# Kernel tuning notes

Measured on AMD Instinct MI355X. Metric: run time of the kernel, lower is better.

The kernel has to match this reference:

```python
import jax, jax.numpy as jnp
import numpy as np

NUM_NODES = 100000
NUM_EDGES = 3200000
N_PER = 400            # nodes per graph (equal-size graphs)
NUM_GRAPHS = 250
K = 100                # sort-pooling k
DIM = 32
IN_DIM = 128
TOTAL = 3 * DIM + 1    # 97 = concat channel count
GDIM = 128
OUT_DIM = 2
DENSE_DIM = (((K - 2) // 2 + 1) - 5 + 1) * 64  # 46*64 = 2944


def setup_inputs() -> dict:
    key = jax.random.key(0)
    ks = jax.random.split(key, 12)

    def lin(k, shape, fan_in):
        return jax.random.normal(k, shape, jnp.float32) / np.float32(np.sqrt(fan_in))

    return {
        "x": jax.random.normal(ks[0], (NUM_NODES, IN_DIM), jnp.float32),
        "edge_index": jax.random.randint(ks[1], (2, NUM_EDGES), 0, NUM_NODES, dtype=jnp.int32),
        "batch": jnp.arange(NUM_NODES, dtype=jnp.int32) // N_PER,
        "W1": lin(ks[2], (IN_DIM, DIM), IN_DIM), "b1": jnp.zeros((DIM,), jnp.float32),
        "W2": lin(ks[3], (DIM, DIM), DIM),       "b2": jnp.zeros((DIM,), jnp.float32),
        "W3": lin(ks[4], (DIM, DIM), DIM),       "b3": jnp.zeros((DIM,), jnp.float32),
        "W4": lin(ks[5], (DIM, 1), DIM),         "b4": jnp.zeros((1,), jnp.float32),
        "cw1": lin(ks[6], (128, 1, TOTAL), TOTAL),   "cb1": jnp.zeros((128,), jnp.float32),
        "cw2": lin(ks[7], (64, 128, 5), 128 * 5),    "cb2": jnp.zeros((64,), jnp.float32),
        "fw1": lin(ks[8], (GDIM, DENSE_DIM), DENSE_DIM), "fb1": jnp.zeros((GDIM,), jnp.float32),
        "fw3": lin(ks[9], (OUT_DIM, GDIM), GDIM),        "fb3": jnp.zeros((OUT_DIM,), jnp.float32),
    }


def _gcn(h_in, W, b, src, dst, coef, deg_inv):
    # GCNConv (improved=False): D^{-1/2}(A+I)D^{-1/2} (h W) + b
    h = h_in @ W
    agg = jax.ops.segment_sum(h[src] * coef, dst, num_segments=NUM_NODES)
    return agg + h * deg_inv[:, None] + b  # deg_inv = self-loop norm dis[i]^2


def reference(x, edge_index, batch, W1, b1, W2, b2, W3, b3, W4, b4,
              cw1, cb1, cw2, cb2, fw1, fb1, fw3, fb3):
    src, dst = edge_index[0], edge_index[1]
    deg = jax.ops.segment_sum(jnp.ones((NUM_EDGES,), x.dtype), dst, num_segments=NUM_NODES) + 1.0
    dis = jax.lax.rsqrt(deg)
    coef = (dis[src] * dis[dst])[:, None]
    deg_inv = 1.0 / deg

    x1 = jnp.tanh(_gcn(x,  W1, b1, src, dst, coef, deg_inv))
    x2 = jnp.tanh(_gcn(x1, W2, b2, src, dst, coef, deg_inv))
    x3 = jnp.tanh(_gcn(x2, W3, b3, src, dst, coef, deg_inv))
    x4 = jnp.tanh(_gcn(x2, W4, b4, src, dst, coef, deg_inv))  # NB: conv4 consumes x2 (as in source)
    xc = jnp.concatenate([x1, x2, x3, x4], axis=1)  # [N, 97]

    # global_sort_pool: per-graph descending sort by last channel, keep top K nodes
    order = jnp.lexsort((-xc[:, -1], batch))  # primary: graph id, secondary: -last channel
    xs = xc[order].reshape(NUM_GRAPHS, N_PER, TOTAL)[:, :K]  # [B, K, 97]

    # Conv1d(1, 128, kernel=stride=97) over flattened [B,1,K*97] == per-slot linear map
    c1 = jax.nn.relu(jnp.einsum('bkt,ct->bck', xs, cw1[:, 0, :]) + cb1[None, :, None])  # [B,128,K]
    p1 = c1.reshape(NUM_GRAPHS, 128, K // 2, 2).max(axis=-1)  # MaxPool1d(2,2) -> [B,128,50]
    c2 = jax.lax.conv_general_dilated(p1, cw2, (1,), 'VALID',
                                      dimension_numbers=('NCH', 'OIH', 'NCH'))
    c2 = jax.nn.relu(c2 + cb2[None, :, None])  # [B,64,46]

    flat = c2.reshape(NUM_GRAPHS, -1)            # [B, 2944]
    h = jax.nn.relu(flat @ fw1.T + fb1)          # fc1 + relu (dropout = identity in eval)
    logits = h @ fw3.T + fb3                     # fc3
    return jax.nn.log_softmax(logits, axis=-1)
```

## Files before the change

### kernel.cpp

```cpp
#include <hip/hip_runtime.h>
#include <hip/hip_bf16.h>

#define NNODES 100000
#define NEDGES 3200000
#define NPADE  4000000
#define NPER   400
#define NGRAPH 250
#define KTOP   100
#define DIM    32
#define INDIM  128
#define TOTALC 97
#define BSHIFT 7
#define BNODES 128
#define NBUCK  782
#define NCHUNK 200
#define CHSZ   16000

__device__ __forceinline__ float bf(unsigned short u) {
    return __uint_as_float(((unsigned)u) << 16);
}
__device__ __forceinline__ unsigned short f2bf(float f) {
    unsigned u = __float_as_uint(f);
    unsigned r = ((u >> 16) & 1u) + 0x7FFFu;
    return (unsigned short)((u + r) >> 16);
}

#define OW_W1   0
#define OW_B1   4096
#define OW_W2   4128
#define OW_B2   5152
#define OW_W3   5184
#define OW_B3   6208
#define OW_W4   6240
#define OW_B4   6272
#define OW_CW1  6280
#define OW_CB1  18696
#define OW_CW2  18824
#define OW_CB2  59784
#define OW_FW1  59848
#define OW_FB1  436680
#define OW_FW3  436808
#define OW_FB3  437064
#define OW_TOT  437072

struct Srcs { const void* p[16]; };

__global__ void k_setup(const unsigned int* __restrict__ xw, Srcs sr,
                        float* __restrict__ dst, float* __restrict__ fw1t,
                        float* __restrict__ w2t8, int* __restrict__ flag) {
    __shared__ int cs[256];
    int t = threadIdx.x;
    int c = 0;
    for (int i = t; i < 4096; i += 256) {
        unsigned e = (xw[i] >> 23) & 0xFFu;
        if (e >= 100u && e <= 150u) c++;
    }
    cs[t] = c;
    __syncthreads();
    for (int off = 128; off > 0; off >>= 1) {
        if (t < off) cs[t] += cs[t + off];
        __syncthreads();
    }
    int isb = (cs[0] < 2048) ? 1 : 0;
    if (blockIdx.x == 0 && t == 0) flag[0] = isb;
    long idx = (long)blockIdx.x * 256 + t;
    if (idx < OW_TOT) {
        const int st[16] = {OW_W1, OW_B1, OW_W2, OW_B2, OW_W3, OW_B3, OW_W4, OW_B4,
                            OW_CW1, OW_CB1, OW_CW2, OW_CB2, OW_FW1, OW_FB1, OW_FW3, OW_FB3};
        const int nn[16] = {4096, 32, 1024, 32, 1024, 32, 32, 1,
                            12416, 128, 40960, 64, 376832, 128, 256, 2};
        #pragma unroll
        for (int s = 0; s < 16; s++) {
            if (idx >= st[s] && idx < st[s] + nn[s]) {
                int l = (int)idx - st[s];
                dst[idx] = isb ? bf(((const unsigned short*)sr.p[s])[l])
                               : ((const float*)sr.p[s])[l];
            }
        }
    } else if (idx < OW_TOT + 376832) {
        int i2 = (int)(idx - OW_TOT);
        float v = isb ? bf(((const unsigned short*)sr.p[12])[i2])
                      : ((const float*)sr.p[12])[i2];
        int j = i2 / 2944, d = i2 - j * 2944;
        fw1t[d * 128 + j] = v;
    } else if (idx < OW_TOT + 376832 + 65536) {
        int k = (int)(idx - OW_TOT - 376832);
        int q = k & 7;
        int co = k >> 3;
        int cc = co >> 6, o = co & 63;
        float v = 0.f;
        if (q < 5) {
            int si = (o * 128 + cc) * 5 + q;
            v = isb ? bf(((const unsigned short*)sr.p[10])[si])
                    : ((const float*)sr.p[10])[si];
        }
        w2t8[k] = v;
    }
}


__global__ __launch_bounds__(1024) void k_hist(const int* __restrict__ ei, int* __restrict__ ghist) {
    __shared__ int h[NBUCK];
    int c = blockIdx.x, t = threadIdx.x;
    for (int i = t; i < NBUCK; i += 1024) h[i] = 0;
    __syncthreads();
    int base = c * CHSZ;
    for (int e = base + t; e < base + CHSZ; e += 1024)
        atomicAdd(&h[ei[NEDGES + e] >> BSHIFT], 1);
    __syncthreads();
    for (int i = t; i < NBUCK; i += 1024) ghist[i * NCHUNK + c] = h[i];
}

__global__ __launch_bounds__(256) void k_scanChunk(int* __restrict__ ghist, int* __restrict__ bcnt) {
    __shared__ int s[256];
    int b = blockIdx.x, t = threadIdx.x;
    int v = (t < NCHUNK) ? ghist[b * NCHUNK + t] : 0;
    s[t] = v;
    __syncthreads();
    for (int o = 1; o < 256; o <<= 1) {
        int u = (t >= o) ? s[t - o] : 0;
        __syncthreads();
        s[t] += u;
        __syncthreads();
    }
    if (t < NCHUNK) ghist[b * NCHUNK + t] = s[t] - v;
    if (t == NCHUNK - 1) bcnt[b] = s[t];
}

__global__ void k_scanB(const int* __restrict__ bcnt, int* __restrict__ boff) {
    __shared__ int s[1024];
    int t = threadIdx.x;
    int v = (t < NBUCK) ? bcnt[t] : 0;
    s[t] = v;
    __syncthreads();
    for (int o = 1; o < 1024; o <<= 1) {
        int u = (t >= o) ? s[t - o] : 0;
        __syncthreads();
        s[t] += u;
        __syncthreads();
    }
    if (t < NBUCK) boff[t] = s[t] - v;
}

__global__ __launch_bounds__(1024) void k_binwrite(const int* __restrict__ ei, const int* __restrict__ boff,
                           const int* __restrict__ ghist, unsigned* __restrict__ staged) {
    __shared__ int cur[NBUCK];
    int c = blockIdx.x, t = threadIdx.x;
    for (int i = t; i < NBUCK; i += 1024) cur[i] = boff[i] + ghist[i * NCHUNK + c];
    __syncthreads();
    int base = c * CHSZ;
    for (int e = base + t; e < base + CHSZ; e += 1024) {
        int s = ei[e], d = ei[NEDGES + e];
        int b = d >> BSHIFT;
        int pos = atomicAdd(&cur[b], 1);
        staged[pos] = ((unsigned)(d & (BNODES - 1)) << 17) | (unsigned)s;
    }
}

__global__ __launch_bounds__(256) void k_nodecnt(const unsigned* __restrict__ staged,
                          const int* __restrict__ boff, int* __restrict__ degi) {
    __shared__ int cnt[BNODES];
    int b = blockIdx.x, t = threadIdx.x;
    if (t < BNODES) cnt[t] = 0;
    __syncthreads();
    int s0 = boff[b];
    int s1 = (b + 1 < NBUCK) ? boff[b + 1] : NEDGES;
    for (int i = s0 + t; i < s1; i += 256)
        atomicAdd(&cnt[staged[i] >> 17], 1);
    __syncthreads();
    int n0 = b << BSHIFT;
    int nn = min(BNODES, NNODES - n0);
    if (t < nn) degi[n0 + t] = cnt[t];
}

__global__ void k_bsum(const int* __restrict__ degi, float* __restrict__ dis,
                       float* __restrict__ dinv, int* __restrict__ bsums) {
    __shared__ int s[256];
    int t = threadIdx.x;
    int i = blockIdx.x * 256 + t;
    int dg = (i < NNODES) ? degi[i] : 0;
    if (i < NNODES) {
        float d = (float)(dg + 1);
        dis[i]  = rsqrtf(d);
        dinv[i] = 1.0f / d;
    }
    s[t] = (i < NNODES) ? ((dg + 7) & ~7) : 0;
    __syncthreads();
    for (int off = 128; off > 0; off >>= 1) {
        if (t < off) s[t] += s[t + off];
        __syncthreads();
    }
    if (t == 0) bsums[blockIdx.x] = s[0];
}

__global__ void k_scanb(int* __restrict__ bsums, int nb) {
    __shared__ int s[512];
    int t = threadIdx.x;
    int v = (t < nb) ? bsums[t] : 0;
    s[t] = v;
    __syncthreads();
    for (int off = 1; off < 512; off <<= 1) {
        int u = (t >= off) ? s[t - off] : 0;
        __syncthreads();
        s[t] += u;
        __syncthreads();
    }
    if (t < nb) bsums[t] = s[t] - v;
}

__global__ void k_scanf(const int* __restrict__ degi, const int* __restrict__ bsums,
                        int* __restrict__ row_off) {
    __shared__ int s[256];
    int t = threadIdx.x;
    int i = blockIdx.x * 256 + t;
    int v = (i < NNODES) ? ((degi[i] + 7) & ~7) : 0;
    s[t] = v;
    __syncthreads();
    for (int off = 1; off < 256; off <<= 1) {
        int u = (t >= off) ? s[t - off] : 0;
        __syncthreads();
        s[t] += u;
        __syncthreads();
    }
    if (i < NNODES) row_off[i] = bsums[blockIdx.x] + s[t] - v;
}

__global__ __launch_bounds__(256) void k_csrfix(const unsigned* __restrict__ staged,
                         const int* __restrict__ boff, const int* __restrict__ row_off,
                         const float* __restrict__ dis,
                         int* __restrict__ csr_src, float* __restrict__ csr_cf) {
    __shared__ int cnt[BNODES];
    __shared__ int rofs[BNODES];
    __shared__ float disl[BNODES];
    int b = blockIdx.x, t = threadIdx.x;
    int n0 = b << BSHIFT;
    int nn = min(BNODES, NNODES - n0);
    if (t < BNODES) {
        cnt[t]  = 0;
        rofs[t] = (t < nn) ? row_off[n0 + t] : 0;
        disl[t] = (t < nn) ? dis[n0 + t] : 0.f;
    }
    __syncthreads();
    int s0 = boff[b];
    int s1 = (b + 1 < NBUCK) ? boff[b + 1] : NEDGES;
    for (int i = s0 + t; i < s1; i += 256) {
        unsigned rec = staged[i];
        int dl = rec >> 17, s = rec & 0x1FFFF;
        int r = atomicAdd(&cnt[dl], 1);
        int slot = rofs[dl] + r;
        csr_src[slot] = s;
        csr_cf[slot]  = dis[s] * disl[dl];
    }
    __syncthreads();
    if (t < nn) {
        int d = cnt[t], dp = (d + 7) & ~7;
        for (int s2 = d; s2 < dp; s2++) {
            csr_src[rofs[t] + s2] = 0;
            csr_cf[rofs[t] + s2]  = 0.f;
        }
    }
}


__global__ void k_mm1(const void* __restrict__ xraw, const float* __restrict__ W1f,
                      const int* __restrict__ flag, float* __restrict__ h) {
    __shared__ float w[INDIM * DIM];
    __shared__ float xsh[8 * INDIM];
    int t = threadIdx.x;
    for (int i = t; i < INDIM * DIM; i += 256) w[i] = W1f[i];
    if (flag[0]) {
        const unsigned int* xsrc = (const unsigned int*)((const unsigned short*)xraw
                                   + (size_t)blockIdx.x * 8 * INDIM);
        for (int i = t; i < 512; i += 256) {
            unsigned u = xsrc[i];
            xsh[2 * i]     = __uint_as_float(u << 16);
            xsh[2 * i + 1] = __uint_as_float(u & 0xFFFF0000u);
        }
    } else {
        const float4* xsrc = (const float4*)((const float*)xraw + (size_t)blockIdx.x * 8 * INDIM);
        float4* xdst = (float4*)xsh;
        for (int i = t; i < 256; i += 256) xdst[i] = xsrc[i];
    }
    __syncthreads();
    int ln = t >> 5, c = t & 31;
    const float* xr = xsh + ln * INDIM;
    float acc = 0.f;
    #pragma unroll 8
    for (int j = 0; j < INDIM; j++) acc += xr[j] * w[j * DIM + c];
    h[(size_t)blockIdx.x * 256 + t] = acc;
}

__global__ void k_gather(const float* __restrict__ xin, const float* __restrict__ h4in,
                         const int* __restrict__ csr_src, const float* __restrict__ csr_cf,
                         const int* __restrict__ row_off, const int* __restrict__ degi,
                         const float* __restrict__ dinv,
                         const float* __restrict__ Wm,
                         const float* __restrict__ bias,
                         const float* __restrict__ w4v,
                         const float* __restrict__ b4,
                         float* __restrict__ xout, float* __restrict__ x4out,
                         float* __restrict__ h4out) {
    __shared__ float wsh[DIM * DIM];
    __shared__ float w4sh[DIM];
    __shared__ float zsh[8 * DIM];
    __shared__ float osh[8 * DIM];
    int t = threadIdx.x;
    if (Wm)  for (int i = t; i < DIM * DIM; i += 256) wsh[i] = Wm[i];
    if (w4v && t < DIM) w4sh[t] = w4v[t];
    int node = blockIdx.x * 8 + (t >> 5);
    int lane = t & 31;
    int wg   = t >> 5;
    int start = row_off[node];
    int cnt   = degi[node];
    int iters = (cnt + 7) >> 3;
    const int4*   ip = (const int4*)(csr_src + start);
    const float4* cp = (const float4*)(csr_cf + start);
    float acc0 = 0.f, acc1 = 0.f;
    if (iters > 0) {
        int4   iA = ip[0], iB = ip[1];
        float4 cA = cp[0], cB = cp[1];
        for (int k = 1; k < iters; k++) {
            int4   nA = ip[2 * k],     nB = ip[2 * k + 1];
            float4 dA = cp[2 * k],     dB = cp[2 * k + 1];
            acc0 += xin[(size_t)iA.x * DIM + lane] * cA.x;
            acc1 += xin[(size_t)iA.y * DIM + lane] * cA.y;
            acc0 += xin[(size_t)iA.z * DIM + lane] * cA.z;
            acc1 += xin[(size_t)iA.w * DIM + lane] * cA.w;
            acc0 += xin[(size_t)iB.x * DIM + lane] * cB.x;
            acc1 += xin[(size_t)iB.y * DIM + lane] * cB.y;
            acc0 += xin[(size_t)iB.z * DIM + lane] * cB.z;
            acc1 += xin[(size_t)iB.w * DIM + lane] * cB.w;
            iA = nA; iB = nB; cA = dA; cB = dB;
        }
        acc0 += xin[(size_t)iA.x * DIM + lane] * cA.x;
        acc1 += xin[(size_t)iA.y * DIM + lane] * cA.y;
        acc0 += xin[(size_t)iA.z * DIM + lane] * cA.z;
        acc1 += xin[(size_t)iA.w * DIM + lane] * cA.w;
        acc0 += xin[(size_t)iB.x * DIM + lane] * cB.x;
        acc1 += xin[(size_t)iB.y * DIM + lane] * cB.y;
        acc0 += xin[(size_t)iB.z * DIM + lane] * cB.z;
        acc1 += xin[(size_t)iB.w * DIM + lane] * cB.w;
    }
    float di = dinv[node];
    float z = acc0 + acc1 + xin[(size_t)node * DIM + lane] * di;
    if (!Wm) {
        xout[(size_t)node * DIM + lane] = tanhf(z + bias[lane]);
    } else {
        zsh[wg * DIM + lane] = z;
        __syncthreads();
        const float* zr = zsh + wg * DIM;
        float a = bias[lane];
        #pragma unroll
        for (int j = 0; j < DIM; j++) a += zr[j] * wsh[j * DIM + lane];
        float outv = tanhf(a);
        xout[(size_t)node * DIM + lane] = outv;
        if (h4out) {
            osh[wg * DIM + lane] = outv;
            __syncthreads();
            if (lane == 0) {
                const float* xr = osh + wg * DIM;
                float a4 = 0.f;
                #pragma unroll
                for (int j = 0; j < DIM; j++) a4 += xr[j] * w4sh[j];
                h4out[node] = a4;
            }
        }
    }
    if (h4in) {
        int cntp = iters << 3;
        float a4 = 0.f;
        for (int ee = lane; ee < cntp; ee += 32)
            a4 += h4in[csr_src[start + ee]] * csr_cf[start + ee];
        for (int off = 16; off > 0; off >>= 1) a4 += __shfl_xor(a4, off, 32);
        if (lane == 0) x4out[node] = tanhf(a4 + h4in[node] * di + b4[0]);
    }
}

__global__ __launch_bounds__(1024) void
k_sortconv1(const float* __restrict__ x1, const float* __restrict__ x2,
            const float* __restrict__ x3, const float* __restrict__ x4,
            const float* __restrict__ cw1f, const float* __restrict__ cb1f,
            float* __restrict__ p1g) {
    __shared__ unsigned long long keys[512];
    __shared__ __align__(16) float xs[32 * 100];
    __shared__ __align__(16) float ws[32 * 128];
    __shared__ int nsh[KTOP];
    int g = blockIdx.x, t = threadIdx.x;
    for (int i = t; i < 512; i += 1024) {
        unsigned long long kk = 0xFFFFFFFFFFFFFFFFULL;
        if (i < NPER) {
            unsigned u = __float_as_uint(x4[g * NPER + i]);
            u = (u & 0x80000000u) ? ~u : (u | 0x80000000u);
            kk = ((unsigned long long)(~u) << 32) | (unsigned)i;
        }
        keys[i] = kk;
    }
    __syncthreads();
    for (int k = 2; k <= 512; k <<= 1)
        for (int j = k >> 1; j > 0; j >>= 1) {
            for (int i = t; i < 512; i += 1024) {
                int l = i ^ j;
                if (l > i) {
                    unsigned long long a = keys[i], b = keys[l];
                    bool asc = ((i & k) == 0);
                    if ((a > b) == asc) { keys[i] = b; keys[l] = a; }
                }
            }
            __syncthreads();
        }
    if (t < KTOP) nsh[t] = g * NPER + (int)(unsigned)(keys[t] & 0xFFFFFFFFu);
    int ct = (t & 31) * 4;
    int kt = (t >> 5) * 4;
    bool act = (t < 800);
    float acc[4][4] = {};
    for (int ch = 0; ch < 3; ch++) {
        const float* arr = (ch == 0) ? x1 : (ch == 1) ? x2 : x3;
        __syncthreads();
        for (int i = t; i < 3200; i += 1024) {
            int q = i & 31, k = i >> 5;
            xs[q * 100 + k] = arr[(size_t)nsh[k] * 32 + q];
        }
        for (int i = t; i < 4096; i += 1024) {
            int c = i & 127, q = i >> 7;
            ws[q * 128 + c] = cw1f[c * TOTALC + ch * 32 + q];
        }
        __syncthreads();
        if (act) {
            for (int q = 0; q < 32; q++) {
                float4 wv = *(const float4*)&ws[q * 128 + ct];
                float4 xv = *(const float4*)&xs[q * 100 + kt];
                float xa[4] = { xv.x, xv.y, xv.z, xv.w };
                float wa[4] = { wv.x, wv.y, wv.z, wv.w };
                #pragma unroll
                for (int a = 0; a < 4; a++)
                    #pragma unroll
                    for (int b = 0; b < 4; b++)
                        acc[a][b] += xa[a] * wa[b];
            }
        }
    }
    if (act) {
        float wa[4];
        #pragma unroll
        for (int b = 0; b < 4; b++) wa[b] = cw1f[(ct + b) * TOTALC + 96];
        #pragma unroll
        for (int a = 0; a < 4; a++) {
            float xv = x4[nsh[kt + a]];
            #pragma unroll
            for (int b = 0; b < 4; b++) acc[a][b] += xv * wa[b];
        }
        int jbase = kt >> 1;
        #pragma unroll
        for (int b = 0; b < 4; b++) {
            float bias = cb1f[ct + b];
            float m0 = fmaxf(fmaxf(acc[0][b], acc[1][b]) + bias, 0.f);
            float m1 = fmaxf(fmaxf(acc[2][b], acc[3][b]) + bias, 0.f);
            p1g[((size_t)g * 128 + ct + b) * 50 + jbase]     = m0;
            p1g[((size_t)g * 128 + ct + b) * 50 + jbase + 1] = m1;
        }
    }
}

__global__ __launch_bounds__(512) void
k_conv2(const float* __restrict__ p1g, const float* __restrict__ w2t8,
        const float* __restrict__ cb2f, float* __restrict__ flatg) {
    __shared__ __align__(16) float p1s[128 * 52];
    __shared__ float fl[64 * 25];
    int bid = blockIdx.x;
    int g = bid >> 1, ph = bid & 1;
    int t = threadIdx.x;
    int p0 = ph ? 24 : 0;
    int np = ph ? 22 : 24;
    for (int i = t; i < 128 * 50; i += 512) {
        int c = i / 50, p = i % 50;
        p1s[c * 52 + p] = p1g[(size_t)g * 6400 + i];
    }
    for (int i = t; i < 128 * 2; i += 512) {
        int c = i >> 1;
        p1s[c * 52 + 50 + (i & 1)] = 0.f;
    }
    for (int i = t; i < 64 * 25; i += 512) fl[i] = 0.f;
    __syncthreads();
    {
        int o = t & 63;
        int c8 = t >> 6;
        float acc[24];
        #pragma unroll
        for (int p = 0; p < 24; p++) acc[p] = 0.f;
        int cbeg = c8 * 16;
        for (int c = cbeg; c < cbeg + 16; c++) {
            const float4* wb = (const float4*)(w2t8 + (((size_t)c * 64 + o) << 3));
            float4 wA = wb[0], wB = wb[1];
            float w0 = wA.x, w1 = wA.y, w2 = wA.z, w3 = wA.w, w4 = wB.x;
            float win[28];
            const float4* wsrc = (const float4*)&p1s[c * 52 + p0];
            #pragma unroll
            for (int v = 0; v < 7; v++) {
                float4 f = wsrc[v];
                win[4 * v] = f.x; win[4 * v + 1] = f.y; win[4 * v + 2] = f.z; win[4 * v + 3] = f.w;
            }
            #pragma unroll
            for (int p = 0; p < 24; p++)
                acc[p] += win[p] * w0 + win[p + 1] * w1 + win[p + 2] * w2
                        + win[p + 3] * w3 + win[p + 4] * w4;
        }
        for (int p = 0; p < np; p++) atomicAdd(&fl[o * 25 + p], acc[p]);
    }
    __syncthreads();
    for (int i = t; i < 64 * 24; i += 512) {
        int o = i / 24, p = i - o * 24;
        if (p < np)
            flatg[(size_t)g * 2944 + o * 46 + p0 + p] = fmaxf(fl[o * 25 + p] + cb2f[o], 0.f);
    }
}

__global__ __launch_bounds__(1024) void
k_fc1(const float* __restrict__ flatg, const float* __restrict__ fw1t,
      float* __restrict__ hpart) {
    __shared__ float fls[5 * 368];
    __shared__ float hp[8 * 5 * 128];
    int b = blockIdx.x;
    int gt = b >> 3, kt = b & 7;
    int t = threadIdx.x;
    int g0 = gt * 5;
    int d0 = kt * 368;
    for (int i = t; i < 5 * 368; i += 1024) {
        int g = i / 368, dd = i - g * 368;
        fls[i] = flatg[(size_t)(g0 + g) * 2944 + d0 + dd];
    }
    __syncthreads();
    int og = t & 127, s8 = t >> 7;
    int ds = s8 * 46;
    const float* wp = fw1t + (size_t)(d0 + ds) * 128 + og;
    const float* f0 = fls + ds;
    float a0 = 0.f, a1 = 0.f, a2 = 0.f, a3 = 0.f, a4 = 0.f;
    #pragma unroll 2
    for (int d = 0; d < 46; d++) {
        float w = wp[(size_t)d * 128];
        a0 += f0[d]            * w;
        a1 += f0[368 + d]      * w;
        a2 += f0[2 * 368 + d]  * w;
        a3 += f0[3 * 368 + d]  * w;
        a4 += f0[4 * 368 + d]  * w;
    }
    hp[(s8 * 5 + 0) * 128 + og] = a0;
    hp[(s8 * 5 + 1) * 128 + og] = a1;
    hp[(s8 * 5 + 2) * 128 + og] = a2;
    hp[(s8 * 5 + 3) * 128 + og] = a3;
    hp[(s8 * 5 + 4) * 128 + og] = a4;
    __syncthreads();
    if (t < 640) {
        int g = t >> 7, o2 = t & 127;
        float s = 0.f;
        #pragma unroll
        for (int s2 = 0; s2 < 8; s2++) s += hp[(s2 * 5 + g) * 128 + o2];
        hpart[((size_t)kt * NGRAPH + g0 + g) * 128 + o2] = s;
    }
}

__global__ void k_fc3(const float* __restrict__ hpart, const float* __restrict__ fb1f,
                      const float* __restrict__ fw3f, const float* __restrict__ fb3f,
                      const int* __restrict__ flag, void* __restrict__ outp) {
    __shared__ float hsh[128];
    int g = blockIdx.x, t = threadIdx.x;
    float s = fb1f[t];
    #pragma unroll
    for (int kt = 0; kt < 8; kt++) s += hpart[((size_t)kt * NGRAPH + g) * 128 + t];
    hsh[t] = fmaxf(s, 0.f);
    __syncthreads();
    if (t < 64) {
        float h0 = hsh[t], h1 = hsh[t + 64];
        float l0 = h0 * fw3f[t] + h1 * fw3f[t + 64];
        float l1 = h0 * fw3f[128 + t] + h1 * fw3f[192 + t];
        #pragma unroll
        for (int off = 32; off > 0; off >>= 1) {
            l0 += __shfl_down(l0, off, 64);
            l1 += __shfl_down(l1, off, 64);
        }
        if (t == 0) {
            l0 += fb3f[0]; l1 += fb3f[1];
            float m = fmaxf(l0, l1);
            float lse = m + logf(expf(l0 - m) + expf(l1 - m));
            if (flag[0]) {
                unsigned short* ob = (unsigned short*)outp;
                ob[g * 2 + 0] = f2bf(l0 - lse);
                ob[g * 2 + 1] = f2bf(l1 - lse);
            } else {
                float* of = (float*)outp;
                of[g * 2 + 0] = l0 - lse;
                of[g * 2 + 1] = l1 - lse;
            }
        }
    }
}


extern "C" void kernel_launch(void* const* d_in, const int* in_sizes, int n_in,
                              void* d_out, int out_size, void* d_ws, size_t ws_size,
                              hipStream_t stream) {
    const void* x  = d_in[0];
    const int* ei  = (const int*)d_in[1];

    char* p = (char*)d_ws;
    auto alloc = [&](size_t bytes) -> void* {
        void* r = (void*)p;
        p += (bytes + 255) & ~(size_t)255;
        return r;
    };
    int*      flag    = (int*)alloc(256);
    float*    wcv     = (float*)alloc((size_t)OW_TOT * 4);
    float*    fw1t    = (float*)alloc((size_t)376832 * 4);
    int*      ghist   = (int*)alloc((size_t)NBUCK * NCHUNK * 4);
    int*      bcnt    = (int*)alloc(1024 * 4);
    int*      boff    = (int*)alloc(1024 * 4);
    int*      bsums   = (int*)alloc(512 * 4);
    int*      degi    = (int*)alloc((size_t)NNODES * 4);
    int*      row_off = (int*)alloc((size_t)NNODES * 4);
    float*    dis     = (float*)alloc((size_t)NNODES * 4);
    float*    dinv    = (float*)alloc((size_t)NNODES * 4);
    unsigned* staged  = (unsigned*)alloc((size_t)NEDGES * 4);
    int*      csr_src = (int*)alloc((size_t)NPADE * 4);
    float*    csr_cf  = (float*)alloc((size_t)NPADE * 4);
    float*    hbuf    = (float*)alloc((size_t)NNODES * DIM * 4);
    float*    h4buf   = (float*)alloc((size_t)NNODES * 4);
    float*    x1      = (float*)alloc((size_t)NNODES * DIM * 4);
    float*    x2      = (float*)alloc((size_t)NNODES * DIM * 4);
    float*    x3      = (float*)alloc((size_t)NNODES * DIM * 4);
    float*    x4      = (float*)alloc((size_t)NNODES * 4);
    float*    p1g     = (float*)alloc((size_t)NGRAPH * 128 * 50 * 4);
    float*    w2t     = (float*)alloc((size_t)64 * 128 * 8 * 4);
    float*    flatg   = (float*)alloc((size_t)NGRAPH * 2944 * 4);
    float*    hpart   = (float*)alloc((size_t)8 * NGRAPH * 128 * 4);
    (void)in_sizes; (void)n_in; (void)out_size; (void)ws_size;

    Srcs sr;
    for (int i = 0; i < 16; i++) sr.p[i] = d_in[3 + i];
    k_setup<<<3436, 256, 0, stream>>>((const unsigned int*)x, sr, wcv, fw1t, w2t, flag);

    k_hist     <<<NCHUNK, 1024, 0, stream>>>(ei, ghist);
    k_scanChunk<<<NBUCK, 256, 0, stream>>>(ghist, bcnt);
    k_scanB    <<<1, 1024, 0, stream>>>(bcnt, boff);
    k_binwrite <<<NCHUNK, 1024, 0, stream>>>(ei, boff, ghist, staged);
    k_nodecnt  <<<NBUCK, 256, 0, stream>>>(staged, boff, degi);
    k_bsum     <<<391, 256, 0, stream>>>(degi, dis, dinv, bsums);
    k_scanb    <<<1, 512, 0, stream>>>(bsums, 391);
    k_scanf    <<<391, 256, 0, stream>>>(degi, bsums, row_off);
    k_csrfix   <<<NBUCK, 256, 0, stream>>>(staged, boff, row_off, dis, csr_src, csr_cf);

    k_mm1   <<<12500, 256, 0, stream>>>(x, wcv + OW_W1, flag, hbuf);
    k_gather<<<12500, 256, 0, stream>>>(hbuf, nullptr, csr_src, csr_cf, row_off, degi, dinv,
                                        nullptr, wcv + OW_B1, nullptr, nullptr,
                                        x1, nullptr, nullptr);
    k_gather<<<12500, 256, 0, stream>>>(x1, nullptr, csr_src, csr_cf, row_off, degi, dinv,
                                        wcv + OW_W2, wcv + OW_B2, wcv + OW_W4, nullptr,
                                        x2, nullptr, h4buf);
    k_gather<<<12500, 256, 0, stream>>>(x2, h4buf, csr_src, csr_cf, row_off, degi, dinv,
                                        wcv + OW_W3, wcv + OW_B3, nullptr, wcv + OW_B4,
                                        x3, x4, nullptr);

    k_sortconv1<<<NGRAPH, 1024, 0, stream>>>(x1, x2, x3, x4, wcv + OW_CW1, wcv + OW_CB1, p1g);
    k_conv2    <<<2 * NGRAPH, 512, 0, stream>>>(p1g, w2t, wcv + OW_CB2, flatg);
    k_fc1      <<<400, 1024, 0, stream>>>(flatg, fw1t, hpart);
    k_fc3      <<<NGRAPH, 128, 0, stream>>>(hpart, wcv + OW_FB1, wcv + OW_FW3, wcv + OW_FB3,
                                            flag, d_out);
}
```

Baseline: 580.6 us.

## Fold GCN edge coefficients into pre-scaled features and drop per-edge coefficient array

Factors the symmetric normalisation dis[src]*dis[dst] out of the edge loop by storing node features pre-scaled by dis[src] and multiplying by dis[dst] after aggregation. The per-edge coefficient array is removed, so each gather reads only source indices. Padding slots now point to an extra zero row instead of carrying a zero weight. The degree/row-offset scans are merged into the bucket kernels, which cuts several launches. In exchange, sort-pool has to undo the scaling with a stored sqrt(deg) for x1 and x2, which adds small rounding differences.

Result: faster. 525.8 us (median of 2 runs) (-9.4%).

```diff
diff --git a/kernel.cpp b/kernel.cpp
--- a/kernel.cpp
+++ b/kernel.cpp
@@ -47,7 +47,9 @@
 
 __global__ void k_setup(const unsigned int* __restrict__ xw, Srcs sr,
                         float* __restrict__ dst, float* __restrict__ fw1t,
-                        float* __restrict__ w2t8, int* __restrict__ flag) {
+                        float* __restrict__ w2t8, int* __restrict__ flag,
+                        float* __restrict__ hb, float* __restrict__ x1b,
+                        float* __restrict__ x2b, float* __restrict__ h4b) {
     __shared__ int cs[256];
     int t = threadIdx.x;
     int c = 0;
@@ -62,7 +64,15 @@
         __syncthreads();
     }
     int isb = (cs[0] < 2048) ? 1 : 0;
-    if (blockIdx.x == 0 && t == 0) flag[0] = isb;
+    if (blockIdx.x == 0) {
+        if (t == 0) flag[0] = isb;
+        if (t < 32) {
+            hb[(size_t)NNODES * DIM + t]  = 0.f;
+            x1b[(size_t)NNODES * DIM + t] = 0.f;
+            x2b[(size_t)NNODES * DIM + t] = 0.f;
+        }
+        if (t == 32) h4b[NNODES] = 0.f;
+    }
     long idx = (long)blockIdx.x * 256 + t;
     if (idx < OW_TOT) {
         const int st[16] = {OW_W1, OW_B1, OW_W2, OW_B2, OW_W3, OW_B3, OW_W4, OW_B4,
@@ -127,10 +137,10 @@
     if (t == NCHUNK - 1) bcnt[b] = s[t];
 }
 
-__global__ void k_scanB(const int* __restrict__ bcnt, int* __restrict__ boff) {
+__global__ void k_scanB(const int* __restrict__ in, int* __restrict__ out) {
     __shared__ int s[1024];
     int t = threadIdx.x;
-    int v = (t < NBUCK) ? bcnt[t] : 0;
+    int v = (t < NBUCK) ? in[t] : 0;
     s[t] = v;
     __syncthreads();
     for (int o = 1; o < 1024; o <<= 1) {
@@ -139,7 +149,7 @@
         s[t] += u;
         __syncthreads();
     }
-    if (t < NBUCK) boff[t] = s[t] - v;
+    if (t < NBUCK) out[t] = s[t] - v;
 }
 
 __global__ __launch_bounds__(1024) void k_binwrite(const int* __restrict__ ei, const int* __restrict__ boff,
@@ -158,8 +168,11 @@
 }
 
 __global__ __launch_bounds__(256) void k_nodecnt(const unsigned* __restrict__ staged,
-                          const int* __restrict__ boff, int* __restrict__ degi) {
+                          const int* __restrict__ boff, int* __restrict__ degi,
+                          float* __restrict__ dis, float* __restrict__ rdis,
+                          int* __restrict__ bucksum) {
     __shared__ int cnt[BNODES];
+    __shared__ int ps[256];
     int b = blockIdx.x, t = threadIdx.x;
     if (t < BNODES) cnt[t] = 0;
     __syncthreads();
@@ -170,76 +183,43 @@
     __syncthreads();
     int n0 = b << BSHIFT;
     int nn = min(BNODES, NNODES - n0);
-    if (t < nn) degi[n0 + t] = cnt[t];
-}
-
-__global__ void k_bsum(const int* __restrict__ degi, float* __restrict__ dis,
-                       float* __restrict__ dinv, int* __restrict__ bsums) {
-    __shared__ int s[256];
-    int t = threadIdx.x;
-    int i = blockIdx.x * 256 + t;
-    int dg = (i < NNODES) ? degi[i] : 0;
-    if (i < NNODES) {
+    int dg = (t < nn) ? cnt[t] : 0;
+    if (t < nn) {
+        degi[n0 + t] = dg;
         float d = (float)(dg + 1);
-        dis[i]  = rsqrtf(d);
-        dinv[i] = 1.0f / d;
-    }
-    s[t] = (i < NNODES) ? ((dg + 7) & ~7) : 0;
+        dis[n0 + t]  = rsqrtf(d);
+        rdis[n0 + t] = sqrtf(d);
+    }
+    ps[t] = (t < nn) ? ((dg + 7) & ~7) : 0;
     __syncthreads();
     for (int off = 128; off > 0; off >>= 1) {
-        if (t < off) s[t] += s[t + off];
-        __syncthreads();
-    }
-    if (t == 0) bsums[blockIdx.x] = s[0];
-}
-
-__global__ void k_scanb(int* __restrict__ bsums, int nb) {
-    __shared__ int s[512];
-    int t = threadIdx.x;
-    int v = (t < nb) ? bsums[t] : 0;
-    s[t] = v;
-    __syncthreads();
-    for (int off = 1; off < 512; off <<= 1) {
-        int u = (t >= off) ? s[t - off] : 0;
-        __syncthreads();
-        s[t] += u;
-        __syncthreads();
-    }
-    if (t < nb) bsums[t] = s[t] - v;
-}
-
-__global__ void k_scanf(const int* __restrict__ degi, const int* __restrict__ bsums,
-                        int* __restrict__ row_off) {
-    __shared__ int s[256];
-    int t = threadIdx.x;
-    int i = blockIdx.x * 256 + t;
-    int v = (i < NNODES) ? ((degi[i] + 7) & ~7) : 0;
-    s[t] = v;
-    __syncthreads();
-    for (int off = 1; off < 256; off <<= 1) {
-        int u = (t >= off) ? s[t - off] : 0;
-        __syncthreads();
-        s[t] += u;
-        __syncthreads();
-    }
-    if (i < NNODES) row_off[i] = bsums[blockIdx.x] + s[t] - v;
+        if (t < off) ps[t] += ps[t + off];
+        __syncthreads();
+    }
+    if (t == 0) bucksum[b] = ps[0];
 }
 
 __global__ __launch_bounds__(256) void k_csrfix(const unsigned* __restrict__ staged,
-                         const int* __restrict__ boff, const int* __restrict__ row_off,
-                         const float* __restrict__ dis,
-                         int* __restrict__ csr_src, float* __restrict__ csr_cf) {
+                         const int* __restrict__ boff, const int* __restrict__ buckoff,
+                         const int* __restrict__ degi,
+                         int* __restrict__ csr_src, int* __restrict__ row_off) {
     __shared__ int cnt[BNODES];
+    __shared__ int sc[BNODES];
     __shared__ int rofs[BNODES];
-    __shared__ float disl[BNODES];
     int b = blockIdx.x, t = threadIdx.x;
     int n0 = b << BSHIFT;
     int nn = min(BNODES, NNODES - n0);
-    if (t < BNODES) {
-        cnt[t]  = 0;
-        rofs[t] = (t < nn) ? row_off[n0 + t] : 0;
-        disl[t] = (t < nn) ? dis[n0 + t] : 0.f;
-    }
+    int pd = (t < nn) ? ((degi[n0 + t] + 7) & ~7) : 0;
+    if (t < BNODES) { cnt[t] = 0; sc[t] = pd; }
+    __syncthreads();
+    for (int o = 1; o < BNODES; o <<= 1) {
+        int u = (t >= o && t < BNODES) ? sc[t - o] : 0;
+        __syncthreads();
+        if (t < BNODES) sc[t] += u;
+        __syncthreads();
+    }
+    if (t < BNODES) rofs[t] = buckoff[b] + sc[t] - pd;
+    if (t < nn) row_off[n0 + t] = rofs[t];
     __syncthreads();
     int s0 = boff[b];
     int s1 = (b + 1 < NBUCK) ? boff[b + 1] : NEDGES;
@@ -247,23 +227,19 @@
         unsigned rec = staged[i];
         int dl = rec >> 17, s = rec & 0x1FFFF;
         int r = atomicAdd(&cnt[dl], 1);
-        int slot = rofs[dl] + r;
-        csr_src[slot] = s;
-        csr_cf[slot]  = dis[s] * disl[dl];
+        csr_src[rofs[dl] + r] = s;
     }
     __syncthreads();
     if (t < nn) {
         int d = cnt[t], dp = (d + 7) & ~7;
-        for (int s2 = d; s2 < dp; s2++) {
-            csr_src[rofs[t] + s2] = 0;
-            csr_cf[rofs[t] + s2]  = 0.f;
-        }
+        for (int s2 = d; s2 < dp; s2++) csr_src[rofs[t] + s2] = NNODES;
     }
 }
 
 
 __global__ void k_mm1(const void* __restrict__ xraw, const float* __restrict__ W1f,
-                      const int* __restrict__ flag, float* __restrict__ h) {
+                      const int* __restrict__ flag, const float* __restrict__ dis,
+                      float* __restrict__ h) {
     __shared__ float w[INDIM * DIM];
     __shared__ float xsh[8 * INDIM];
     int t = threadIdx.x;
@@ -287,19 +263,20 @@
     float acc = 0.f;
     #pragma unroll 8
     for (int j = 0; j < INDIM; j++) acc += xr[j] * w[j * DIM + c];
-    h[(size_t)blockIdx.x * 256 + t] = acc;
-}
-
-__global__ void k_gather(const float* __restrict__ xin, const float* __restrict__ h4in,
-                         const int* __restrict__ csr_src, const float* __restrict__ csr_cf,
+    int node = blockIdx.x * 8 + ln;
+    h[(size_t)node * DIM + c] = acc * dis[node];
+}
+
+__global__ void k_gather(const float* __restrict__ xin, const float* __restrict__ h4s,
+                         const int* __restrict__ csr_src,
                          const int* __restrict__ row_off, const int* __restrict__ degi,
-                         const float* __restrict__ dinv,
+                         const float* __restrict__ dis,
                          const float* __restrict__ Wm,
                          const float* __restrict__ bias,
                          const float* __restrict__ w4v,
                          const float* __restrict__ b4,
                          float* __restrict__ xout, float* __restrict__ x4out,
-                         float* __restrict__ h4out) {
+                         float* __restrict__ h4out, int scaleOut) {
     __shared__ float wsh[DIM * DIM];
     __shared__ float w4sh[DIM];
     __shared__ float zsh[8 * DIM];
@@ -313,38 +290,36 @@
     int start = row_off[node];
     int cnt   = degi[node];
     int iters = (cnt + 7) >> 3;
-    const int4*   ip = (const int4*)(csr_src + start);
-    const float4* cp = (const float4*)(csr_cf + start);
+    const int4* ip = (const int4*)(csr_src + start);
     float acc0 = 0.f, acc1 = 0.f;
     if (iters > 0) {
-        int4   iA = ip[0], iB = ip[1];
-        float4 cA = cp[0], cB = cp[1];
+        int4 iA = ip[0], iB = ip[1];
         for (int k = 1; k < iters; k++) {
-            int4   nA = ip[2 * k],     nB = ip[2 * k + 1];
-            float4 dA = cp[2 * k],     dB = cp[2 * k + 1];
-            acc0 += xin[(size_t)iA.x * DIM + lane] * cA.x;
-            acc1 += xin[(size_t)iA.y * DIM + lane] * cA.y;
-            acc0 += xin[(size_t)iA.z * DIM + lane] * cA.z;
-            acc1 += xin[(size_t)iA.w * DIM + lane] * cA.w;
-            acc0 += xin[(size_t)iB.x * DIM + lane] * cB.x;
-            acc1 += xin[(size_t)iB.y * DIM + lane] * cB.y;
-            acc0 += xin[(size_t)iB.z * DIM + lane] * cB.z;
-            acc1 += xin[(size_t)iB.w * DIM + lane] * cB.w;
-            iA = nA; iB = nB; cA = dA; cB = dB;
-        }
-        acc0 += xin[(size_t)iA.x * DIM + lane] * cA.x;
-        acc1 += xin[(size_t)iA.y * DIM + lane] * cA.y;
-        acc0 += xin[(size_t)iA.z * DIM + lane] * cA.z;
-        acc1 += xin[(size_t)iA.w * DIM + lane] * cA.w;
-        acc0 += xin[(size_t)iB.x * DIM + lane] * cB.x;
-        acc1 += xin[(size_t)iB.y * DIM + lane] * cB.y;
-        acc0 += xin[(size_t)iB.z * DIM + lane] * cB.z;
-        acc1 += xin[(size_t)iB.w * DIM + lane] * cB.w;
-    }
-    float di = dinv[node];
-    float z = acc0 + acc1 + xin[(size_t)node * DIM + lane] * di;
+            int4 nA = ip[2 * k], nB = ip[2 * k + 1];
+            acc0 += xin[(size_t)iA.x * DIM + lane];
+            acc1 += xin[(size_t)iA.y * DIM + lane];
+            acc0 += xin[(size_t)iA.z * DIM + lane];
+            acc1 += xin[(size_t)iA.w * DIM + lane];
+            acc0 += xin[(size_t)iB.x * DIM + lane];
+            acc1 += xin[(size_t)iB.y * DIM + lane];
+            acc0 += xin[(size_t)iB.z * DIM + lane];
+            acc1 += xin[(size_t)iB.w * DIM + lane];
+            iA = nA; iB = nB;
+        }
+        acc0 += xin[(size_t)iA.x * DIM + lane];
+        acc1 += xin[(size_t)iA.y * DIM + lane];
+        acc0 += xin[(size_t)iA.z * DIM + lane];
+        acc1 += xin[(size_t)iA.w * DIM + lane];
+        acc0 += xin[(size_t)iB.x * DIM + lane];
+        acc1 += xin[(size_t)iB.y * DIM + lane];
+        acc0 += xin[(size_t)iB.z * DIM + lane];
+        acc1 += xin[(size_t)iB.w * DIM + lane];
+    }
+    float disv = dis[node];
+    float z = (acc0 + acc1 + xin[(size_t)node * DIM + lane]) * disv;
     if (!Wm) {
-        xout[(size_t)node * DIM + lane] = tanhf(z + bias[lane]);
+        float outv = tanhf(z + bias[lane]);
+        xout[(size_t)node * DIM + lane] = outv * disv;
     } else {
         zsh[wg * DIM + lane] = z;
         __syncthreads();
@@ -353,7 +328,7 @@
         #pragma unroll
         for (int j = 0; j < DIM; j++) a += zr[j] * wsh[j * DIM + lane];
         float outv = tanhf(a);
-        xout[(size_t)node * DIM + lane] = outv;
+        xout[(size_t)node * DIM + lane] = scaleOut ? outv * disv : outv;
         if (h4out) {
             osh[wg * DIM + lane] = outv;
             __syncthreads();
@@ -362,29 +337,31 @@
                 float a4 = 0.f;
                 #pragma unroll
                 for (int j = 0; j < DIM; j++) a4 += xr[j] * w4sh[j];
-                h4out[node] = a4;
+                h4out[node] = a4 * disv;
             }
         }
     }
-    if (h4in) {
+    if (h4s) {
         int cntp = iters << 3;
         float a4 = 0.f;
         for (int ee = lane; ee < cntp; ee += 32)
-            a4 += h4in[csr_src[start + ee]] * csr_cf[start + ee];
+            a4 += h4s[csr_src[start + ee]];
         for (int off = 16; off > 0; off >>= 1) a4 += __shfl_xor(a4, off, 32);
-        if (lane == 0) x4out[node] = tanhf(a4 + h4in[node] * di + b4[0]);
+        if (lane == 0) x4out[node] = tanhf((a4 + h4s[node]) * disv + b4[0]);
     }
 }
 
 __global__ __launch_bounds__(1024) void
 k_sortconv1(const float* __restrict__ x1, const float* __restrict__ x2,
             const float* __restrict__ x3, const float* __restrict__ x4,
+            const float* __restrict__ rdis,
             const float* __restrict__ cw1f, const float* __restrict__ cb1f,
             float* __restrict__ p1g) {
     __shared__ unsigned long long keys[512];
     __shared__ __align__(16) float xs[32 * 100];
     __shared__ __align__(16) float ws[32 * 128];
     __shared__ int nsh[KTOP];
+    __shared__ float rdl[KTOP];
     int g = blockIdx.x, t = threadIdx.x;
     for (int i = t; i < 512; i += 1024) {
         unsigned long long kk = 0xFFFFFFFFFFFFFFFFULL;
@@ -408,7 +385,11 @@
             }
             __syncthreads();
         }
-    if (t < KTOP) nsh[t] = g * NPER + (int)(unsigned)(keys[t] & 0xFFFFFFFFu);
+    if (t < KTOP) {
+        int nid = g * NPER + (int)(unsigned)(keys[t] & 0xFFFFFFFFu);
+        nsh[t] = nid;
+        rdl[t] = rdis[nid];
+    }
     int ct = (t & 31) * 4;
     int kt = (t >> 5) * 4;
     bool act = (t < 800);
@@ -418,7 +399,9 @@
         __syncthreads();
         for (int i = t; i < 3200; i += 1024) {
             int q = i & 31, k = i >> 5;
-            xs[q * 100 + k] = arr[(size_t)nsh[k] * 32 + q];
+            float v = arr[(size_t)nsh[k] * 32 + q];
+            if (ch < 2) v *= rdl[k];
+            xs[q * 100 + k] = v;
         }
         for (int i = t; i < 4096; i += 1024) {
             int c = i & 127, q = i >> 7;
@@ -613,18 +596,18 @@
     int*      ghist   = (int*)alloc((size_t)NBUCK * NCHUNK * 4);
     int*      bcnt    = (int*)alloc(1024 * 4);
     int*      boff    = (int*)alloc(1024 * 4);
-    int*      bsums   = (int*)alloc(512 * 4);
+    int*      bucksum = (int*)alloc(1024 * 4);
+    int*      buckoff = (int*)alloc(1024 * 4);
     int*      degi    = (int*)alloc((size_t)NNODES * 4);
     int*      row_off = (int*)alloc((size_t)NNODES * 4);
     float*    dis     = (float*)alloc((size_t)NNODES * 4);
-    float*    dinv    = (float*)alloc((size_t)NNODES * 4);
+    float*    rdis    = (float*)alloc((size_t)NNODES * 4);
     unsigned* staged  = (unsigned*)alloc((size_t)NEDGES * 4);
     int*      csr_src = (int*)alloc((size_t)NPADE * 4);
-    float*    csr_cf  = (float*)alloc((size_t)NPADE * 4);
-    float*    hbuf    = (float*)alloc((size_t)NNODES * DIM * 4);
-    float*    h4buf   = (float*)alloc((size_t)NNODES * 4);
-    float*    x1      = (float*)alloc((size_t)NNODES * DIM * 4);
-    float*    x2      = (float*)alloc((size_t)NNODES * DIM * 4);
+    float*    hbuf    = (float*)alloc(((size_t)NNODES * DIM + 256) * 4);
+    float*    h4buf   = (float*)alloc(((size_t)NNODES + 256) * 4);
+    float*    x1      = (float*)alloc(((size_t)NNODES * DIM + 256) * 4);
+    float*    x2      = (float*)alloc(((size_t)NNODES * DIM + 256) * 4);
     float*    x3      = (float*)alloc((size_t)NNODES * DIM * 4);
     float*    x4      = (float*)alloc((size_t)NNODES * 4);
     float*    p1g     = (float*)alloc((size_t)NGRAPH * 128 * 50 * 4);
@@ -635,30 +618,30 @@
 
     Srcs sr;
     for (int i = 0; i < 16; i++) sr.p[i] = d_in[3 + i];
-    k_setup<<<3436, 256, 0, stream>>>((const unsigned int*)x, sr, wcv, fw1t, w2t, flag);
+    k_setup<<<3436, 256, 0, stream>>>((const unsigned int*)x, sr, wcv, fw1t, w2t, flag,
+                                      hbuf, x1, x2, h4buf);
 
     k_hist     <<<NCHUNK, 1024, 0, stream>>>(ei, ghist);
     k_scanChunk<<<NBUCK, 256, 0, stream>>>(ghist, bcnt);
     k_scanB    <<<1, 1024, 0, stream>>>(bcnt, boff);
     k_binwrite <<<NCHUNK, 1024, 0, stream>>>(ei, boff, ghist, staged);
-    k_nodecnt  <<<NBUCK, 256, 0, stream>>>(staged, boff, degi);
-    k_bsum     <<<391, 256, 0, stream>>>(degi, dis, dinv, bsums);
-    k_scanb    <<<1, 512, 0, stream>>>(bsums, 391);
-    k_scanf    <<<391, 256, 0, stream>>>(degi, bsums, row_off);
-    k_csrfix   <<<NBUCK, 256, 0, stream>>>(staged, boff, row_off, dis, csr_src, csr_cf);
-
-    k_mm1   <<<12500, 256, 0, stream>>>(x, wcv + OW_W1, flag, hbuf);
-    k_gather<<<12500, 256, 0, stream>>>(hbuf, nullptr, csr_src, csr_cf, row_off, degi, dinv,
+    k_nodecnt  <<<NBUCK, 256, 0, stream>>>(staged, boff, degi, dis, rdis, bucksum);
+    k_scanB    <<<1, 1024, 0, stream>>>(bucksum, buckoff);
+    k_csrfix   <<<NBUCK, 256, 0, stream>>>(staged, boff, buckoff, degi, csr_src, row_off);
+
+    k_mm1   <<<12500, 256, 0, stream>>>(x, wcv + OW_W1, flag, dis, hbuf);
+    k_gather<<<12500, 256, 0, stream>>>(hbuf, nullptr, csr_src, row_off, degi, dis,
                                         nullptr, wcv + OW_B1, nullptr, nullptr,
-                                        x1, nullptr, nullptr);
-    k_gather<<<12500, 256, 0, stream>>>(x1, nullptr, csr_src, csr_cf, row_off, degi, dinv,
+                                        x1, nullptr, nullptr, 1);
+    k_gather<<<12500, 256, 0, stream>>>(x1, nullptr, csr_src, row_off, degi, dis,
                                         wcv + OW_W2, wcv + OW_B2, wcv + OW_W4, nullptr,
-                                        x2, nullptr, h4buf);
-    k_gather<<<12500, 256, 0, stream>>>(x2, h4buf, csr_src, csr_cf, row_off, degi, dinv,
+                                        x2, nullptr, h4buf, 1);
+    k_gather<<<12500, 256, 0, stream>>>(x2, h4buf, csr_src, row_off, degi, dis,
                                         wcv + OW_W3, wcv + OW_B3, nullptr, wcv + OW_B4,
-                                        x3, x4, nullptr);
-
-    k_sortconv1<<<NGRAPH, 1024, 0, stream>>>(x1, x2, x3, x4, wcv + OW_CW1, wcv + OW_CB1, p1g);
+                                        x3, x4, nullptr, 0);
+
+    k_sortconv1<<<NGRAPH, 1024, 0, stream>>>(x1, x2, x3, x4, rdis,
+                                             wcv + OW_CW1, wcv + OW_CB1, p1g);
     k_conv2    <<<2 * NGRAPH, 512, 0, stream>>>(p1g, w2t, wcv + OW_CB2, flatg);
     k_fc1      <<<400, 1024, 0, stream>>>(flatg, fw1t, hpart);
     k_fc3      <<<NGRAPH, 128, 0, stream>>>(hpart, wcv + OW_FB1, wcv + OW_FW3, wcv + OW_FB3,
```
